# Kernel tuning notes

Measured on AMD Instinct MI355X. Metric: run time of the kernel, lower is better.

## Reference

```python
import jax, jax.numpy as jnp
import numpy as np

EPS = 1e-5

def conv3x3(x, w, bias=None):
    y = jax.lax.conv_general_dilated(x, w, (1, 1), 'SAME',
                                     dimension_numbers=('NCHW', 'OIHW', 'NCHW'))
    if bias is not None:
        y = y + bias[None, :, None, None]
    return y

def batchnorm(x, g, b):
    m = x.mean((0, 2, 3), keepdims=True)
    v = x.var((0, 2, 3), keepdims=True)
    return (x - m) * jax.lax.rsqrt(v + EPS) * g[None, :, None, None] + b[None, :, None, None]

def deform_sample(x, offset, mask, dg=2):
    # x: [B,C,H,W]; offset: [B,dg*9*2,H,W] (dy,dx interleaved per mmcv); mask: [B,dg*9,H,W]
    B, C, H, W = x.shape
    K = 9
    cg = C // dg
    off = offset.reshape(B, dg, K, 2, H, W)
    dy, dx = off[:, :, :, 0], off[:, :, :, 1]
    m = mask.reshape(B, dg, K, H, W)
    ky = (jnp.repeat(jnp.arange(3), 3) - 1).astype(x.dtype)   # kernel row offset per tap
    kx = (jnp.tile(jnp.arange(3), 3) - 1).astype(x.dtype)     # kernel col offset per tap
    py = dy + jnp.arange(H, dtype=x.dtype)[None, None, None, :, None] + ky[None, None, :, None, None]
    px = dx + jnp.arange(W, dtype=x.dtype)[None, None, None, None, :] + kx[None, None, :, None, None]
    y0 = jnp.floor(py); x0 = jnp.floor(px)
    ly = py - y0; lx = px - x0
    y0i = y0.astype(jnp.int32); x0i = x0.astype(jnp.int32)
    y1i = y0i + 1; x1i = x0i + 1
    def ok(yy, xx):
        return ((yy >= 0) & (yy < H) & (xx >= 0) & (xx < W)).astype(x.dtype)
    xg = x.reshape(B, dg, cg, H * W)
    def gather(yy, xx):
        idx = (jnp.clip(yy, 0, H - 1) * W + jnp.clip(xx, 0, W - 1)).reshape(B, dg, -1)
        g = jax.vmap(jax.vmap(lambda im, ii: im[:, ii]))(xg, idx)   # [B,dg,cg,K*H*W]
        return g.reshape(B, dg, cg, K, H, W)
    w00 = ((1 - ly) * (1 - lx) * ok(y0i, x0i))[:, :, None]
    w01 = ((1 - ly) * lx * ok(y0i, x1i))[:, :, None]
    w10 = (ly * (1 - lx) * ok(y1i, x0i))[:, :, None]
    w11 = (ly * lx * ok(y1i, x1i))[:, :, None]
    val = (gather(y0i, x0i) * w00 + gather(y0i, x1i) * w01 +
           gather(y1i, x0i) * w10 + gather(y1i, x1i) * w11)
    return val * m[:, :, None]   # [B,dg,cg,K,H,W]

def reference(input_v, input_i, off_w, off_b, dconv_w, bn1_g, bn1_b, conv2_w, bn2_g, bn2_b):
    x = jnp.concatenate([input_v, input_i], axis=1)             # [B,C,H,W]
    off_all = conv3x3(x, off_w, off_b)                          # [B,54,H,W]
    o1, o2, mask = jnp.split(off_all, 3, axis=1)
    offset = jnp.concatenate([o1, o2], axis=1)                  # [B,36,H,W]
    mask = jax.nn.sigmoid(mask)                                 # [B,18,H,W]
    sampled = deform_sample(x, offset, mask, dg=2)              # [B,2,cg,9,H,W]
    O = dconv_w.shape[0]
    out = jnp.einsum('bgckhw,ogck->bohw', sampled, dconv_w.reshape(O, 2, -1, 9))
    out = jax.nn.relu(batchnorm(out, bn1_g, bn1_b))
    out = jax.nn.relu(batchnorm(conv3x3(out, conv2_w), bn2_g, bn2_b))
    return out

def setup_inputs() -> dict:
    key = jax.random.key(0)
    ks = jax.random.split(key, 8)
    B, Cm, O, H, W = 4, 128, 128, 64, 64
    C = 2 * Cm
    inp = {}
    inp['input_v'] = jax.random.normal(ks[0], (B, Cm, H, W), jnp.float32)
    inp['input_i'] = jax.random.normal(ks[1], (B, Cm, H, W), jnp.float32)
    # offset/mask conv (zero-init in torch; small random here for a non-trivial reference)
    inp['off_w'] = jax.random.normal(ks[2], (54, C, 3, 3), jnp.float32) * 0.02
    inp['off_b'] = jnp.zeros((54,), jnp.float32)
    inp['dconv_w'] = jax.random.normal(ks[3], (O, C, 3, 3), jnp.float32) * (1.0 / np.sqrt(C * 9))
    inp['bn1_g'] = jnp.ones((O,), jnp.float32)
    inp['bn1_b'] = jnp.zeros((O,), jnp.float32)
    inp['conv2_w'] = jax.random.normal(ks[4], (O, O, 3, 3), jnp.float32) * (1.0 / np.sqrt(O * 9))
    inp['bn2_g'] = jnp.ones((O,), jnp.float32)
    inp['bn2_b'] = jnp.zeros((O,), jnp.float32)
    return inp
```

## Files before the change

### kernel.cpp

```cpp
#include <hip/hip_runtime.h>

#define EPSBN 1e-5f

using s8v = __attribute__((ext_vector_type(8))) short;
using f4v = __attribute__((ext_vector_type(4))) float;

__device__ inline unsigned short f2bf(float f) {
  unsigned u = __float_as_uint(f);
  return (unsigned short)((u + 0x7FFFu + ((u >> 16) & 1u)) >> 16);
}

__global__ __launch_bounds__(256) void k_pack(const float* __restrict__ v, const float* __restrict__ im,
                                              unsigned short* __restrict__ xb) {
  __shared__ float tile[64][33];
  int b = blockIdx.z;
  int hw0 = blockIdx.x * 32;
  int c0 = blockIdx.y * 64;
  int tx = threadIdx.x, ty = threadIdx.y;
#pragma unroll
  for (int i = 0; i < 64; i += 8) {
    int c = c0 + ty + i;
    const float* src = (c < 128) ? (v + ((size_t)b * 128 + c) * 4096)
                                 : (im + ((size_t)b * 128 + (c - 128)) * 4096);
    tile[ty + i][tx] = src[hw0 + tx];
  }
  __syncthreads();
#pragma unroll
  for (int i = 0; i < 32; i += 8) {
    int hw = hw0 + ty + i;
    ushort2 o;
    o.x = f2bf(tile[2 * tx][ty + i]);
    o.y = f2bf(tile[2 * tx + 1][ty + i]);
    *(ushort2*)&xb[((size_t)(b * 4096 + hw)) * 256 + c0 + 2 * tx] = o;
  }
}

__global__ __launch_bounds__(256) void k_wprep_all(const float* __restrict__ w_off,
                                                   const float* __restrict__ w_d,
                                                   const float* __restrict__ w_2,
                                                   unsigned short* __restrict__ wt_off,
                                                   unsigned short* __restrict__ wt_d,
                                                   unsigned short* __restrict__ wt_2) {
  int bid = blockIdx.x, t = threadIdx.x;
  if (bid < 72) {
    int id = bid * 256 + t;
    int lane = id & 63;
    int nb = (id >> 6) & 3;
    int ks = id >> 8;
    int ks2 = ks & 1, tap = (ks >> 1) % 9, cc = ks / 18;
    int o = nb * 16 + (lane & 15);
    int cb = cc * 64 + ks2 * 32 + ((lane >> 4) * 8);
    s8v r;
#pragma unroll
    for (int j = 0; j < 8; ++j) {
      float val = (o < 54) ? w_off[((size_t)o * 256 + cb + j) * 9 + tap] : 0.f;
      r[j] = (short)f2bf(val);
    }
    *(s8v*)&wt_off[(size_t)id * 8] = r;
  } else if (bid < 216) {
    int id = (bid - 72) * 256 + t;
    int lane = id & 63;
    int nb = (id >> 6) & 7;
    int kstep = id >> 9;
    int chunk = kstep >> 2, ks4 = kstep & 3;
    int g = chunk / 9, kk = chunk % 9;
    int o = nb * 16 + (lane & 15);
    int cb = g * 128 + ks4 * 32 + ((lane >> 4) * 8);
    s8v r;
#pragma unroll
    for (int j = 0; j < 8; ++j) r[j] = (short)f2bf(w_d[((size_t)o * 256 + cb + j) * 9 + kk]);
    *(s8v*)&wt_d[(size_t)id * 8] = r;
  } else {
    int id = (bid - 216) * 256 + t;
    int lane = id & 63;
    int nb = (id >> 6) & 7;
    int kstep = id >> 9;
    int ks2 = kstep & 1, tap = (kstep >> 1) % 9, cc = kstep / 18;
    int o = nb * 16 + (lane & 15);
    int cb = cc * 64 + ks2 * 32 + ((lane >> 4) * 8);
    s8v r;
#pragma unroll
    for (int j = 0; j < 8; ++j) r[j] = (short)f2bf(w_2[((size_t)o * 128 + cb + j) * 9 + tap]);
    *(s8v*)&wt_2[(size_t)id * 8] = r;
  }
}

__global__ __launch_bounds__(512, 3) void k_offconv(const unsigned short* __restrict__ xb,
                                                    const unsigned short* __restrict__ wt,
                                                    const float* __restrict__ bias,
                                                    float* __restrict__ off) {
  __shared__ char Xs[102 * 512];
  __shared__ float redx[2048];
  int bid = blockIdx.x;
  int id8 = (bid & 7) * 64 + (bid >> 3);
  int w0 = (id8 & 1) * 32;
  int h = (id8 >> 1) & 63;
  int b = id8 >> 7;
  int t = threadIdx.x;
  int l = t & 63, wv = t >> 6;
  int og = wv & 3, kh = wv >> 2;
  f4v zero = {0.f, 0.f, 0.f, 0.f};
  f4v acc[2] = {zero, zero};

  for (int id = t; id < 3264; id += 512) {
    int tr = id >> 5, oq8 = id & 31;
    int ky = tr / 34, col = tr % 34;
    int hh = h + ky - 1, ww = w0 + col - 1;
    s8v val = {0, 0, 0, 0, 0, 0, 0, 0};
    if ((unsigned)hh < 64u && (unsigned)ww < 64u)
      val = *(const s8v*)&xb[(((size_t)(b * 64 + hh)) * 64 + ww) * 256 + oq8 * 8];
    int byte = (tr * 512 + oq8 * 16) ^ ((tr & 7) << 4);
    *(s8v*)(Xs + byte) = val;
  }
  __syncthreads();
  int khi = l >> 4, lo = l & 15;
#pragma unroll
  for (int tap = 0; tap < 9; ++tap) {
    int ky = tap / 3, kx = tap % 3;
#pragma unroll
    for (int s = 0; s < 4; ++s) {
      int cc = kh * 2 + (s >> 1);
      int ks2 = s & 1;
      int kstep = cc * 18 + tap * 2 + ks2;
      int chb = cc * 128 + ks2 * 64 + khi * 16;
      s8v bfr = *(const s8v*)&wt[((size_t)(kstep * 4 + og) * 64 + l) * 8];
#pragma unroll
      for (int m = 0; m < 2; ++m) {
        int tr = ky * 34 + m * 16 + lo + kx;
        int rbyte = (tr * 512 + chb) ^ ((tr & 7) << 4);
        s8v a = *(const s8v*)(Xs + rbyte);
        acc[m] = __builtin_amdgcn_mfma_f32_16x16x32_bf16(a, bfr, acc[m], 0, 0, 0);
      }
    }
  }
  if (kh == 1) {
#pragma unroll
    for (int m = 0; m < 2; ++m)
#pragma unroll
      for (int j = 0; j < 4; ++j) redx[((og * 64 + l) * 2 + m) * 4 + j] = acc[m][j];
  }
  __syncthreads();
  if (kh == 0) {
    int o = og * 16 + lo;
    int pixb = (b * 64 + h) * 64 + w0;
    if (o < 54) {
      float bi = bias[o];
#pragma unroll
      for (int m = 0; m < 2; ++m)
#pragma unroll
        for (int j = 0; j < 4; ++j) {
          int px = pixb + m * 16 + khi * 4 + j;
          float vv = acc[m][j] + redx[((og * 64 + l) * 2 + m) * 4 + j] + bi;
          if (o >= 36) vv = 1.f / (1.f + __expf(-vv));
          off[(size_t)px * 54 + o] = vv;
        }
    }
  }
}

#define DC_ISSUE(c, V, Q)                                   \
  do {                                                      \
    const unsigned* ip_ = sidx[(c)][px];                    \
    const float* qp_ = swt[(c)][px];                        \
    Q##0 = qp_[0]; Q##1 = qp_[1]; Q##2 = qp_[2]; Q##3 = qp_[3]; \
    V##00 = *(const s8v*)&xb[ip_[0] + chof0];               \
    V##01 = *(const s8v*)&xb[ip_[1] + chof0];               \
    V##02 = *(const s8v*)&xb[ip_[2] + chof0];               \
    V##03 = *(const s8v*)&xb[ip_[3] + chof0];               \
    V##10 = *(const s8v*)&xb[ip_[0] + chof1];               \
    V##11 = *(const s8v*)&xb[ip_[1] + chof1];               \
    V##12 = *(const s8v*)&xb[ip_[2] + chof1];               \
    V##13 = *(const s8v*)&xb[ip_[3] + chof1];               \
  } while (0)

#define DC_HALF(c, A0, A1, A2, A3, Q, WB)                               \
  do {                                                                  \
    unsigned rr_[4];                                                    \
    _Pragma("unroll") for (int jp_ = 0; jp_ < 4; ++jp_) {               \
      unsigned w0_ = ((const unsigned*)&A0)[jp_];                       \
      unsigned w1_ = ((const unsigned*)&A1)[jp_];                       \
      unsigned w2_ = ((const unsigned*)&A2)[jp_];                       \
      unsigned w3_ = ((const unsigned*)&A3)[jp_];                       \
      float e_ = Q##0 * __uint_as_float(w0_ << 16) + Q##1 * __uint_as_float(w1_ << 16) + \
                 Q##2 * __uint_as_float(w2_ << 16) + Q##3 * __uint_as_float(w3_ << 16);  \
      float o_ = Q##0 * __uint_as_float(w0_ & 0xffff0000u) + Q##1 * __uint_as_float(w1_ & 0xffff0000u) + \
                 Q##2 * __uint_as_float(w2_ & 0xffff0000u) + Q##3 * __uint_as_float(w3_ & 0xffff0000u);  \
      unsigned p_;                                                      \
      asm("v_cvt_pk_bf16_f32 %0, %1, %2" : "=v"(p_) : "v"(e_), "v"(o_)); \
      rr_[jp_] = p_;                                                    \
    }                                                                   \
    *(int4*)(&At[(c) & 1][0] + (WB)) = *(int4*)rr_;                     \
  } while (0)

#define DC_COMMIT(c, V, Q)                                  \
  do {                                                      \
    DC_HALF(c, V##00, V##01, V##02, V##03, Q, wbyte0);      \
    DC_HALF(c, V##10, V##11, V##12, V##13, Q, wbyte1);      \
  } while (0)

#define LDS_BARRIER()                                        \
  do {                                                       \
    asm volatile("s_waitcnt lgkmcnt(0)" ::: "memory");       \
    __builtin_amdgcn_s_barrier();                            \
  } while (0)

__global__ __launch_bounds__(512, 2) void k_dconv(const unsigned short* __restrict__ xb,
                                                  const float* __restrict__ off,
                                                  const unsigned short* __restrict__ wt,
                                                  float* __restrict__ y1p,
                                                  float* __restrict__ st1, float* __restrict__ st2) {
  __shared__ unsigned int sidx[18][64][4];
  __shared__ float swt[18][64][4];
  __shared__ char At[2][16384];
  int t = threadIdx.x;
  int l = t & 63, og = t >> 6;
  int bid = blockIdx.x;
  int id8 = (bid & 7) * 32 + (bid >> 3);
  int pixb = id8 * 64;
  int b = id8 >> 6, h = id8 & 63;

  for (int id = t; id < 1152; id += 512) {
    int chunk = id >> 6, ppx = id & 63;
    int g = chunk / 9, kk = chunk % 9;
    const float* op = off + (size_t)(pixb + ppx) * 54;
    float dy = op[(g * 9 + kk) * 2];
    float dx = op[(g * 9 + kk) * 2 + 1];
    float msk = op[36 + g * 9 + kk];
    float py = dy + (float)(h + kk / 3 - 1);
    float pxf = dx + (float)(ppx + kk % 3 - 1);
    float y0f = floorf(py), x0f = floorf(pxf);
    float ly = py - y0f, lx = pxf - x0f;
    int y0 = (int)y0f, x0 = (int)x0f;
    int y1 = y0 + 1, x1 = x0 + 1;
    float oky0 = (y0 >= 0 && y0 < 64) ? 1.f : 0.f;
    float oky1 = (y1 >= 0 && y1 < 64) ? 1.f : 0.f;
    float okx0 = (x0 >= 0 && x0 < 64) ? 1.f : 0.f;
    float okx1 = (x1 >= 0 && x1 < 64) ? 1.f : 0.f;
    int y0c = min(max(y0, 0), 63), y1c = min(max(y1, 0), 63);
    int x0c = min(max(x0, 0), 63), x1c = min(max(x1, 0), 63);
    unsigned base = (unsigned)(b * 4096);
    unsigned gofs = (unsigned)(g * 128);
    sidx[chunk][ppx][0] = (base + y0c * 64 + x0c) * 256u + gofs;
    sidx[chunk][ppx][1] = (base + y0c * 64 + x1c) * 256u + gofs;
    sidx[chunk][ppx][2] = (base + y1c * 64 + x0c) * 256u + gofs;
    sidx[chunk][ppx][3] = (base + y1c * 64 + x1c) * 256u + gofs;
    swt[chunk][ppx][0] = (1.f - ly) * (1.f - lx) * oky0 * okx0 * msk;
    swt[chunk][ppx][1] = (1.f - ly) * lx * oky0 * okx1 * msk;
    swt[chunk][ppx][2] = ly * (1.f - lx) * oky1 * okx0 * msk;
    swt[chunk][ppx][3] = ly * lx * oky1 * okx1 * msk;
  }
  __syncthreads();

  int px = t >> 3;
  int cq = t & 7;
  unsigned chof0 = cq * 16u, chof1 = cq * 16u + 8u;
  int wbyte0 = (px * 256 + cq * 32) ^ ((px & 7) << 4);
  int wbyte1 = (px * 256 + cq * 32 + 16) ^ ((px & 7) << 4);
  int khi = l >> 4, lo = l & 15;

  s8v va00, va01, va02, va03, va10, va11, va12, va13;
  s8v vb00, vb01, vb02, vb03, vb10, vb11, vb12, vb13;
  float qa0, qa1, qa2, qa3, qb0, qb1, qb2, qb3;

  DC_ISSUE(0, va, qa);
  DC_ISSUE(1, vb, qb);
  DC_COMMIT(0, va, qa);
  LDS_BARRIER();

  f4v zero = {0.f, 0.f, 0.f, 0.f};
  f4v acc[4] = {zero, zero, zero, zero};

  for (int c = 0; c < 18; ++c) {
    if (c < 16) {
      if ((c & 1) == 0) DC_ISSUE(c + 2, va, qa);
      else              DC_ISSUE(c + 2, vb, qb);
    }
#pragma unroll
    for (int ks4 = 0; ks4 < 4; ++ks4) {
      int kstep = c * 4 + ks4;
      s8v bfr = *(const s8v*)&wt[((size_t)(kstep * 8 + og) * 64 + l) * 8];
      int chb = ks4 * 64 + khi * 16;
#pragma unroll
      for (int m = 0; m < 4; ++m) {
        int trA = m * 16 + lo;
        int rbyte = (trA * 256 + chb) ^ ((trA & 7) << 4);
        s8v a = *(const s8v*)(&At[c & 1][0] + rbyte);
        acc[m] = __builtin_amdgcn_mfma_f32_16x16x32_bf16(a, bfr, acc[m], 0, 0, 0);
      }
    }
    if (c < 17) {
      if ((c & 1) == 0) DC_COMMIT(c + 1, vb, qb);
      else              DC_COMMIT(c + 1, va, qa);
    }
    LDS_BARRIER();
  }

  int o = og * 16 + lo;
  float s1v = 0.f, s2v = 0.f;
#pragma unroll
  for (int m = 0; m < 4; ++m)
#pragma unroll
    for (int j = 0; j < 4; ++j) {
      float vv = acc[m][j];
      y1p[(size_t)(pixb + m * 16 + khi * 4 + j) * 128 + o] = vv;
      s1v += vv; s2v += vv * vv;
    }
  float* red = &swt[0][0][0];
  red[khi * 128 + o] = s1v;
  red[512 + khi * 128 + o] = s2v;
  __syncthreads();
  if (t < 128) {
    float a1 = 0.f, a2 = 0.f;
#pragma unroll
    for (int rr = 0; rr < 4; ++rr) { a1 += red[rr * 128 + t]; a2 += red[512 + rr * 128 + t]; }
    atomicAdd(&st1[t], a1);
    atomicAdd(&st2[t], a2);
  }
}

__global__ __launch_bounds__(256) void k_bnrelu1(const float* __restrict__ yp, const float* __restrict__ s1,
                                                 const float* __restrict__ s2, const float* __restrict__ g,
                                                 const float* __restrict__ bb, unsigned short* __restrict__ yb) {
  __shared__ float sc[128], sh[128];
  int t = threadIdx.x;
  if (t < 128) {
    float m = s1[t] * (1.f / 16384.f);
    float var = s2[t] * (1.f / 16384.f) - m * m;
    float s = g[t] * rsqrtf(var + EPSBN);
    sc[t] = s;
    sh[t] = bb[t] - m * s;
  }
  __syncthreads();
  size_t i = ((size_t)blockIdx.x * 256 + t) * 8;
  int c0 = (int)(i & 127);
  float4 u = *(const float4*)&yp[i];
  float4 v = *(const float4*)&yp[i + 4];
  s8v r;
  r[0] = (short)f2bf(fmaxf(0.f, u.x * sc[c0 + 0] + sh[c0 + 0]));
  r[1] = (short)f2bf(fmaxf(0.f, u.y * sc[c0 + 1] + sh[c0 + 1]));
  r[2] = (short)f2bf(fmaxf(0.f, u.z * sc[c0 + 2] + sh[c0 + 2]));
  r[3] = (short)f2bf(fmaxf(0.f, u.w * sc[c0 + 3] + sh[c0 + 3]));
  r[4] = (short)f2bf(fmaxf(0.f, v.x * sc[c0 + 4] + sh[c0 + 4]));
  r[5] = (short)f2bf(fmaxf(0.f, v.y * sc[c0 + 5] + sh[c0 + 5]));
  r[6] = (short)f2bf(fmaxf(0.f, v.z * sc[c0 + 6] + sh[c0 + 6]));
  r[7] = (short)f2bf(fmaxf(0.f, v.w * sc[c0 + 7] + sh[c0 + 7]));
  *(s8v*)&yb[i] = r;
}

__global__ __launch_bounds__(512, 3) void k_conv2(const unsigned short* __restrict__ yb,
                                                  const unsigned short* __restrict__ wt,
                                                  float* __restrict__ y2p,
                                                  float* __restrict__ st1, float* __restrict__ st2) {
  __shared__ char Bs[102 * 256];
  int bid = blockIdx.x;
  int id8 = (bid & 7) * 64 + (bid >> 3);
  int w0 = (id8 & 1) * 32;
  int h = (id8 >> 1) & 63;
  int b = id8 >> 7;
  int t = threadIdx.x;
  int l = t & 63, og = t >> 6;
  f4v zero = {0.f, 0.f, 0.f, 0.f};
  f4v acc[2] = {zero, zero};

  for (int id = t; id < 1632; id += 512) {
    int tr = id >> 4, oq = id & 15;
    int ky = tr / 34, col = tr % 34;
    int hh = h + ky - 1, ww = w0 + col - 1;
    s8v val = {0, 0, 0, 0, 0, 0, 0, 0};
    if ((unsigned)hh < 64u && (unsigned)ww < 64u)
      val = *(const s8v*)&yb[(((size_t)(b * 64 + hh)) * 64 + ww) * 128 + oq * 8];
    int byte = (tr * 256 + oq * 16) ^ ((tr & 7) << 4);
    *(s8v*)(Bs + byte) = val;
  }
  __syncthreads();
  int khi = l >> 4, lo = l & 15;
#pragma unroll
  for (int tap = 0; tap < 9; ++tap) {
    int ky = tap / 3, kx = tap % 3;
#pragma unroll
    for (int ks4 = 0; ks4 < 4; ++ks4) {
      int kstep = ((ks4 >> 1) * 9 + tap) * 2 + (ks4 & 1);
      s8v bfr = *(const s8v*)&wt[((size_t)(kstep * 8 + og) * 64 + l) * 8];
      int chb = ks4 * 64 + khi * 16;
#pragma unroll
      for (int m = 0; m < 2; ++m) {
        int tr = ky * 34 + m * 16 + lo + kx;
        int rbyte = (tr * 256 + chb) ^ ((tr & 7) << 4);
        s8v a = *(const s8v*)(Bs + rbyte);
        acc[m] = __builtin_amdgcn_mfma_f32_16x16x32_bf16(a, bfr, acc[m], 0, 0, 0);
      }
    }
  }
  __syncthreads();
  int pixb = (b * 64 + h) * 64 + w0;
  int o = og * 16 + lo;
  float s1v = 0.f, s2v = 0.f;
#pragma unroll
  for (int m = 0; m < 2; ++m)
#pragma unroll
    for (int j = 0; j < 4; ++j) {
      float vv = acc[m][j];
      y2p[(size_t)(pixb + m * 16 + khi * 4 + j) * 128 + o] = vv;
      s1v += vv; s2v += vv * vv;
    }
  float* red = (float*)Bs;
  red[khi * 128 + o] = s1v;
  red[512 + khi * 128 + o] = s2v;
  __syncthreads();
  if (t < 128) {
    float a1 = 0.f, a2 = 0.f;
#pragma unroll
    for (int rr = 0; rr < 4; ++rr) { a1 += red[rr * 128 + t]; a2 += red[512 + rr * 128 + t]; }
    atomicAdd(&st1[t], a1);
    atomicAdd(&st2[t], a2);
  }
}

__global__ __launch_bounds__(256) void k_bnrelu2(const float* __restrict__ yp, const float* __restrict__ s1,
                                                 const float* __restrict__ s2, const float* __restrict__ g,
                                                 const float* __restrict__ bb, float* __restrict__ out) {
  __shared__ float sc[128], sh[128];
  __shared__ float buf[64 * 129];
  int t = threadIdx.x;
  if (t < 128) {
    float m = s1[t] * (1.f / 16384.f);
    float var = s2[t] * (1.f / 16384.f) - m * m;
    float s = g[t] * rsqrtf(var + EPSBN);
    sc[t] = s;
    sh[t] = bb[t] - m * s;
  }
  int bh = blockIdx.x;
  int b = bh >> 6, h = bh & 63;
  const float* src = yp + (size_t)bh * 8192;
  for (int i = t; i < 2048; i += 256) {
    float4 v = ((const float4*)src)[i];
    int w = (i * 4) >> 7, o = (i * 4) & 127;
    float* d = &buf[w * 129 + o];
    d[0] = v.x; d[1] = v.y; d[2] = v.z; d[3] = v.w;
  }
  __syncthreads();
  for (int id = t; id < 8192; id += 256) {
    int o = id >> 6, w = id & 63;
    float v = buf[w * 129 + o];
    v = fmaxf(0.f, v * sc[o] + sh[o]);
    out[(((size_t)b * 128 + o) * 64 + h) * 64 + w] = v;
  }
}

extern "C" void kernel_launch(void* const* d_in, const int* in_sizes, int n_in,
                              void* d_out, int out_size, void* d_ws, size_t ws_size,
                              hipStream_t stream) {
  const float* in_v = (const float*)d_in[0];
  const float* in_i = (const float*)d_in[1];
  const float* off_w = (const float*)d_in[2];
  const float* off_b = (const float*)d_in[3];
  const float* dconv_w = (const float*)d_in[4];
  const float* bn1_g = (const float*)d_in[5];
  const float* bn1_b = (const float*)d_in[6];
  const float* conv2_w = (const float*)d_in[7];
  const float* bn2_g = (const float*)d_in[8];
  const float* bn2_b = (const float*)d_in[9];
  float* out = (float*)d_out;

  char* w = (char*)d_ws;
  unsigned short* xb = (unsigned short*)w;      w += (size_t)16384 * 256 * 2;
  float* off_nhwc = (float*)w;                  w += (size_t)16384 * 54 * 4;
  unsigned short* wtf_off = (unsigned short*)w; w += (size_t)18432 * 8 * 2;
  unsigned short* wtf_d = (unsigned short*)w;   w += (size_t)36864 * 8 * 2;
  unsigned short* wtf_2 = (unsigned short*)w;   w += (size_t)18432 * 8 * 2;
  float* y1p = (float*)w;                       w += (size_t)16384 * 128 * 4;
  unsigned short* y1b = (unsigned short*)w;     w += (size_t)16384 * 128 * 2;
  float* y2p = (float*)w;                       w += (size_t)16384 * 128 * 4;
  float* stats = (float*)w;                     w += 512 * 4;

  hipMemsetAsync(stats, 0, 512 * 4, stream);
  k_pack<<<dim3(128, 4, 4), dim3(32, 8), 0, stream>>>(in_v, in_i, xb);
  k_wprep_all<<<288, 256, 0, stream>>>(off_w, dconv_w, conv2_w, wtf_off, wtf_d, wtf_2);
  k_offconv<<<512, 512, 0, stream>>>(xb, wtf_off, off_b, off_nhwc);
  k_dconv<<<256, 512, 0, stream>>>(xb, off_nhwc, wtf_d, y1p, stats, stats + 128);
  k_bnrelu1<<<1024, 256, 0, stream>>>(y1p, stats, stats + 128, bn1_g, bn1_b, y1b);
  k_conv2<<<512, 512, 0, stream>>>(y1b, wtf_2, y2p, stats + 256, stats + 384);
  k_bnrelu2<<<256, 256, 0, stream>>>(y2p, stats + 256, stats + 384, bn2_g, bn2_b, out);
}
```

Measured before the change: 176.3 us.

## Halve dconv pixel tile, triple-buffer A staging, raise occupancy with setprio

The deformable conv kernel now handles 32 pixels per block instead of 64, doubling the grid to 512 blocks and shrinking LDS so launch bounds can request 4 blocks per CU. The A-tile staging moves from double to triple buffering, with gathers issued three chunks ahead, and the MFMA section is wrapped in s_setprio. The aim is to hide gather latency through more prefetch distance and more resident waves. The cost is that each weight fragment is reused across only 2 MFMA row tiles instead of 4, and the B weights are reloaded by twice as many blocks.

After: 166.2 us. 1.06x faster.

```diff
diff --git a/kernel.cpp b/kernel.cpp
--- a/kernel.cpp
+++ b/kernel.cpp
@@ -163,24 +163,20 @@
     const unsigned* ip_ = sidx[(c)][px];                    \
     const float* qp_ = swt[(c)][px];                        \
     Q##0 = qp_[0]; Q##1 = qp_[1]; Q##2 = qp_[2]; Q##3 = qp_[3]; \
-    V##00 = *(const s8v*)&xb[ip_[0] + chof0];               \
-    V##01 = *(const s8v*)&xb[ip_[1] + chof0];               \
-    V##02 = *(const s8v*)&xb[ip_[2] + chof0];               \
-    V##03 = *(const s8v*)&xb[ip_[3] + chof0];               \
-    V##10 = *(const s8v*)&xb[ip_[0] + chof1];               \
-    V##11 = *(const s8v*)&xb[ip_[1] + chof1];               \
-    V##12 = *(const s8v*)&xb[ip_[2] + chof1];               \
-    V##13 = *(const s8v*)&xb[ip_[3] + chof1];               \
+    V##0 = *(const s8v*)&xb[ip_[0] + chof];                 \
+    V##1 = *(const s8v*)&xb[ip_[1] + chof];                 \
+    V##2 = *(const s8v*)&xb[ip_[2] + chof];                 \
+    V##3 = *(const s8v*)&xb[ip_[3] + chof];                 \
   } while (0)
 
-#define DC_HALF(c, A0, A1, A2, A3, Q, WB)                               \
+#define DC_COMMIT(BUF, V, Q)                                            \
   do {                                                                  \
     unsigned rr_[4];                                                    \
     _Pragma("unroll") for (int jp_ = 0; jp_ < 4; ++jp_) {               \
-      unsigned w0_ = ((const unsigned*)&A0)[jp_];                       \
-      unsigned w1_ = ((const unsigned*)&A1)[jp_];                       \
-      unsigned w2_ = ((const unsigned*)&A2)[jp_];                       \
-      unsigned w3_ = ((const unsigned*)&A3)[jp_];                       \
+      unsigned w0_ = ((const unsigned*)&V##0)[jp_];                     \
+      unsigned w1_ = ((const unsigned*)&V##1)[jp_];                     \
+      unsigned w2_ = ((const unsigned*)&V##2)[jp_];                     \
+      unsigned w3_ = ((const unsigned*)&V##3)[jp_];                     \
       float e_ = Q##0 * __uint_as_float(w0_ << 16) + Q##1 * __uint_as_float(w1_ << 16) + \
                  Q##2 * __uint_as_float(w2_ << 16) + Q##3 * __uint_as_float(w3_ << 16);  \
       float o_ = Q##0 * __uint_as_float(w0_ & 0xffff0000u) + Q##1 * __uint_as_float(w1_ & 0xffff0000u) + \
@@ -189,13 +185,7 @@
       asm("v_cvt_pk_bf16_f32 %0, %1, %2" : "=v"(p_) : "v"(e_), "v"(o_)); \
       rr_[jp_] = p_;                                                    \
     }                                                                   \
-    *(int4*)(&At[(c) & 1][0] + (WB)) = *(int4*)rr_;                     \
-  } while (0)
-
-#define DC_COMMIT(c, V, Q)                                  \
-  do {                                                      \
-    DC_HALF(c, V##00, V##01, V##02, V##03, Q, wbyte0);      \
-    DC_HALF(c, V##10, V##11, V##12, V##13, Q, wbyte1);      \
+    *(int4*)(&At[BUF][0] + wbyte) = *(int4*)rr_;                        \
   } while (0)
 
 #define LDS_BARRIER()                                        \
@@ -204,30 +194,55 @@
     __builtin_amdgcn_s_barrier();                            \
   } while (0)
 
-__global__ __launch_bounds__(512, 2) void k_dconv(const unsigned short* __restrict__ xb,
+#define DC_MFMA(C, BUF)                                                 \
+  do {                                                                  \
+    __builtin_amdgcn_s_setprio(1);                                      \
+    _Pragma("unroll") for (int ks4_ = 0; ks4_ < 4; ++ks4_) {            \
+      int kstep_ = (C) * 4 + ks4_;                                      \
+      s8v bfr_ = *(const s8v*)&wt[((size_t)(kstep_ * 8 + og) * 64 + l) * 8]; \
+      int chb_ = ks4_ * 64 + khi * 16;                                  \
+      _Pragma("unroll") for (int m_ = 0; m_ < 2; ++m_) {                \
+        int trA_ = m_ * 16 + lo;                                        \
+        int rbyte_ = (trA_ * 256 + chb_) ^ ((trA_ & 7) << 4);           \
+        s8v a_ = *(const s8v*)(&At[BUF][0] + rbyte_);                   \
+        acc[m_] = __builtin_amdgcn_mfma_f32_16x16x32_bf16(a_, bfr_, acc[m_], 0, 0, 0); \
+      }                                                                 \
+    }                                                                   \
+    __builtin_amdgcn_s_setprio(0);                                      \
+  } while (0)
+
+#define DC_PHASE(C, BUF, VI, QI, VC, QC, BUFC)               \
+  do {                                                       \
+    if ((C) < 15) DC_ISSUE((C) + 3, VI, QI);                 \
+    DC_MFMA(C, BUF);                                         \
+    if ((C) < 17) DC_COMMIT(BUFC, VC, QC);                   \
+    LDS_BARRIER();                                           \
+  } while (0)
+
+__global__ __launch_bounds__(512, 4) void k_dconv(const unsigned short* __restrict__ xb,
                                                   const float* __restrict__ off,
                                                   const unsigned short* __restrict__ wt,
                                                   float* __restrict__ y1p,
                                                   float* __restrict__ st1, float* __restrict__ st2) {
-  __shared__ unsigned int sidx[18][64][4];
-  __shared__ float swt[18][64][4];
-  __shared__ char At[2][16384];
+  __shared__ unsigned int sidx[18][32][4];
+  __shared__ float swt[18][32][4];
+  __shared__ char At[3][8192];
   int t = threadIdx.x;
   int l = t & 63, og = t >> 6;
   int bid = blockIdx.x;
-  int id8 = (bid & 7) * 32 + (bid >> 3);
-  int pixb = id8 * 64;
-  int b = id8 >> 6, h = id8 & 63;
-
-  for (int id = t; id < 1152; id += 512) {
-    int chunk = id >> 6, ppx = id & 63;
+  int id8 = (bid & 7) * 64 + (bid >> 3);
+  int pixb = id8 * 32;
+  int b = pixb >> 12, h = (pixb >> 6) & 63, w0 = pixb & 63;
+
+  for (int id = t; id < 576; id += 512) {
+    int chunk = id >> 5, ppx = id & 31;
     int g = chunk / 9, kk = chunk % 9;
     const float* op = off + (size_t)(pixb + ppx) * 54;
     float dy = op[(g * 9 + kk) * 2];
     float dx = op[(g * 9 + kk) * 2 + 1];
     float msk = op[36 + g * 9 + kk];
     float py = dy + (float)(h + kk / 3 - 1);
-    float pxf = dx + (float)(ppx + kk % 3 - 1);
+    float pxf = dx + (float)(w0 + ppx + kk % 3 - 1);
     float y0f = floorf(py), x0f = floorf(pxf);
     float ly = py - y0f, lx = pxf - x0f;
     int y0 = (int)y0f, x0 = (int)x0f;
@@ -251,54 +266,34 @@
   }
   __syncthreads();
 
-  int px = t >> 3;
-  int cq = t & 7;
-  unsigned chof0 = cq * 16u, chof1 = cq * 16u + 8u;
-  int wbyte0 = (px * 256 + cq * 32) ^ ((px & 7) << 4);
-  int wbyte1 = (px * 256 + cq * 32 + 16) ^ ((px & 7) << 4);
+  int px = t >> 4, oq = t & 15;
+  unsigned chof = oq * 8u;
+  int wbyte = (px * 256 + oq * 16) ^ ((px & 7) << 4);
   int khi = l >> 4, lo = l & 15;
 
-  s8v va00, va01, va02, va03, va10, va11, va12, va13;
-  s8v vb00, vb01, vb02, vb03, vb10, vb11, vb12, vb13;
-  float qa0, qa1, qa2, qa3, qb0, qb1, qb2, qb3;
+  s8v va0, va1, va2, va3, vb0, vb1, vb2, vb3, vc0, vc1, vc2, vc3;
+  float qa0, qa1, qa2, qa3, qb0, qb1, qb2, qb3, qc0, qc1, qc2, qc3;
 
   DC_ISSUE(0, va, qa);
   DC_ISSUE(1, vb, qb);
+  DC_ISSUE(2, vc, qc);
   DC_COMMIT(0, va, qa);
   LDS_BARRIER();
 
   f4v zero = {0.f, 0.f, 0.f, 0.f};
-  f4v acc[4] = {zero, zero, zero, zero};
-
-  for (int c = 0; c < 18; ++c) {
-    if (c < 16) {
-      if ((c & 1) == 0) DC_ISSUE(c + 2, va, qa);
-      else              DC_ISSUE(c + 2, vb, qb);
-    }
-#pragma unroll
-    for (int ks4 = 0; ks4 < 4; ++ks4) {
-      int kstep = c * 4 + ks4;
-      s8v bfr = *(const s8v*)&wt[((size_t)(kstep * 8 + og) * 64 + l) * 8];
-      int chb = ks4 * 64 + khi * 16;
-#pragma unroll
-      for (int m = 0; m < 4; ++m) {
-        int trA = m * 16 + lo;
-        int rbyte = (trA * 256 + chb) ^ ((trA & 7) << 4);
-        s8v a = *(const s8v*)(&At[c & 1][0] + rbyte);
-        acc[m] = __builtin_amdgcn_mfma_f32_16x16x32_bf16(a, bfr, acc[m], 0, 0, 0);
-      }
-    }
-    if (c < 17) {
-      if ((c & 1) == 0) DC_COMMIT(c + 1, vb, qb);
-      else              DC_COMMIT(c + 1, va, qa);
-    }
-    LDS_BARRIER();
+  f4v acc[2] = {zero, zero};
+
+  for (int cb = 0; cb < 6; ++cb) {
+    int c0 = cb * 3;
+    DC_PHASE(c0 + 0, 0, va, qa, vb, qb, 1);
+    DC_PHASE(c0 + 1, 1, vb, qb, vc, qc, 2);
+    DC_PHASE(c0 + 2, 2, vc, qc, va, qa, 0);
   }
 
   int o = og * 16 + lo;
   float s1v = 0.f, s2v = 0.f;
 #pragma unroll
-  for (int m = 0; m < 4; ++m)
+  for (int m = 0; m < 2; ++m)
 #pragma unroll
     for (int j = 0; j < 4; ++j) {
       float vv = acc[m][j];
@@ -477,7 +472,7 @@
   k_pack<<<dim3(128, 4, 4), dim3(32, 8), 0, stream>>>(in_v, in_i, xb);
   k_wprep_all<<<288, 256, 0, stream>>>(off_w, dconv_w, conv2_w, wtf_off, wtf_d, wtf_2);
   k_offconv<<<512, 512, 0, stream>>>(xb, wtf_off, off_b, off_nhwc);
-  k_dconv<<<256, 512, 0, stream>>>(xb, off_nhwc, wtf_d, y1p, stats, stats + 128);
+  k_dconv<<<512, 512, 0, stream>>>(xb, off_nhwc, wtf_d, y1p, stats, stats + 128);
   k_bnrelu1<<<1024, 256, 0, stream>>>(y1p, stats, stats + 128, bn1_g, bn1_b, y1b);
   k_conv2<<<512, 512, 0, stream>>>(y1b, wtf_2, y2p, stats + 256, stats + 384);
   k_bnrelu2<<<256, 256, 0, stream>>>(y2p, stats + 256, stats + 384, bn2_g, bn2_b, out);
```
